# Optimization experiments

Measured on AMD Instinct MI355X. Metric: run time of the kernel, lower is better.

Reference implementation:

```python
import jax, jax.numpy as jnp
import numpy as np
import math

C_CURV = 1.0          # manifold curvature c
KH = KW = 3
STRIDE = (1, 1)
PADDING = (1, 1)
DILATION = (1, 1)
IN_CH = 64            # includes time channel
OUT_CH = 64           # excludes time channel


def setup_inputs() -> dict:
    key = jax.random.key(0)
    k1, k2, k3 = jax.random.split(key, 3)
    B, H, W = 32, 64, 64
    x = jax.random.normal(k1, (B, H, W, IN_CH), dtype=jnp.float32)
    kk = KH * KW
    lin_in = (IN_CH - 1) * kk + 1  # 568
    stdv = math.sqrt(2.0 / ((IN_CH - 1) * kk))
    weight = jax.random.uniform(k2, (OUT_CH, lin_in), minval=-stdv, maxval=stdv, dtype=jnp.float32)
    bias = jax.random.uniform(k3, (OUT_CH,), minval=-stdv, maxval=stdv, dtype=jnp.float32)
    return {"x": x, "weight": weight, "bias": bias}


def _im2col(x):
    """x: [B,H,W,C] -> gathered patches [B,h_out,w_out,KH,KW,C] (torch Unfold semantics)."""
    B, H, W, C = x.shape
    xp = jnp.pad(x, ((0, 0), (PADDING[0], PADDING[0]), (PADDING[1], PADDING[1]), (0, 0)))
    h_out = (H + 2 * PADDING[0] - DILATION[0] * (KH - 1) - 1) // STRIDE[0] + 1
    w_out = (W + 2 * PADDING[1] - DILATION[1] * (KW - 1) - 1) // STRIDE[1] + 1
    rows = STRIDE[0] * jnp.arange(h_out)[:, None] + DILATION[0] * jnp.arange(KH)[None, :]  # [h_out,KH]
    cols = STRIDE[1] * jnp.arange(w_out)[:, None] + DILATION[1] * jnp.arange(KW)[None, :]  # [w_out,KW]
    g = xp[:, rows[:, None, :, None], cols[None, :, None, :], :]  # [B,h_out,w_out,KH,KW,C]
    return g, h_out, w_out


def reference(x, weight, bias):
    B = x.shape[0]
    kk = KH * KW
    g, h_out, w_out = _im2col(x)
    L = h_out * w_out
    # Time channel (channel 0) over kernel positions, clamped to sqrt(c)
    t = jnp.maximum(g[..., 0].reshape(B, L, kk), jnp.sqrt(jnp.float32(C_CURV)))
    t_rescaled = jnp.sqrt(jnp.sum(t * t, axis=-1, keepdims=True) - (kk - 1) * C_CURV)
    # Space channels in kernel-major, channel-minor order (matches torch reshape/transpose)
    s = g[..., 1:].reshape(B, L, kk * (IN_CH - 1))
    feat = jnp.concatenate([t_rescaled, s], axis=-1)  # [B, L, 568]
    # LorentzLinear: linear on features, recompute time from space norm
    y_space = jnp.einsum('blf,of->blo', feat, weight) + bias
    y_time = jnp.sqrt(jnp.sum(y_space * y_space, axis=-1, keepdims=True) + C_CURV)
    out = jnp.concatenate([y_time, y_space], axis=-1)
    return out.reshape(B, h_out, w_out, OUT_CH + 1)
```

## Files before the change

### kernel.cpp

```cpp
#include <hip/hip_runtime.h>
#include <cstdint>
#include <cstddef>

typedef __attribute__((ext_vector_type(8))) short short8v;
typedef __attribute__((ext_vector_type(4))) unsigned uint4v;
typedef __attribute__((ext_vector_type(4))) float floatx4;

#define LIN 568

__device__ __forceinline__ short f32_to_bf16(float f) {
  unsigned u = __builtin_bit_cast(unsigned, f);
  u += 0x7fffu + ((u >> 16) & 1u);
  return (short)(u >> 16);
}
__device__ __forceinline__ float bf16_to_f32(short s) {
  return __builtin_bit_cast(float, ((unsigned)(unsigned short)s) << 16);
}
__device__ __forceinline__ unsigned cvt_pk_bf16(float lo, float hi) {
  unsigned r;
  asm("v_cvt_pk_bf16_f32 %0, %1, %2" : "=v"(r) : "v"(lo), "v"(hi));
  return r;
}

__global__ void prep_weight(const float* __restrict__ w, short* __restrict__ wfragg) {
  int i = blockIdx.x * 256 + threadIdx.x;
  if (i >= 9 * 2 * 4 * 64 * 8) return;
  int j    = i & 7;
  int lane = (i >> 3) & 63;
  int nb   = (i >> 9) & 3;
  int half = (i >> 11) & 1;
  int tap  = i >> 12;
  int n = nb * 16 + (lane & 15);
  int c = half * 32 + ((lane >> 4) << 3) + j;
  float v = (c == 0) ? 0.0f : w[n * LIN + 1 + tap * 63 + (c - 1)];
  wfragg[i] = f32_to_bf16(v);
}

__launch_bounds__(256, 2)
__global__ void lconv_main(const float* __restrict__ x, const float* __restrict__ w,
                           const float* __restrict__ bias, const short* __restrict__ wfragg,
                           float* __restrict__ out) {
  __shared__ short xt[6 * 66 * 72];

  const int tid = threadIdx.x;
  const int bb = blockIdx.x >> 4;
  const int h0 = (blockIdx.x & 15) << 2;
  const float* xb = x + (size_t)bb * (64 * 64 * 64);

  const int lane = tid & 63;
  const int l15 = lane & 15;
  const int q = lane >> 4;
  const int wv = tid >> 6;

  const short* wfl = wfragg + lane * 8;
  short8v b0[4], b1[4], b2[4];
#pragma unroll
  for (int nb = 0; nb < 4; ++nb) {
    b0[nb] = *(const short8v*)(wfl + 0 * 2048 + nb * 512);
    b1[nb] = *(const short8v*)(wfl + 1 * 2048 + nb * 512);
    b2[nb] = *(const short8v*)(wfl + 2 * 2048 + nb * 512);
  }
  float bj[4], w0j[4];
#pragma unroll
  for (int nb = 0; nb < 4; ++nb) {
    int n = nb * 16 + l15;
    bj[nb] = bias[n];
    w0j[nb] = w[n * LIN];
  }

#pragma unroll
  for (int i = 0; i < 8; ++i) {
    int idx = i * 256 + tid;
    int row = idx >> 9;
    int rem = idx & 511;
    int col = rem >> 3;
    int ch8 = (rem & 7) << 3;
    int h = h0 - 1 + row;
    float4 v0 = {0.f, 0.f, 0.f, 0.f}, v1 = {0.f, 0.f, 0.f, 0.f};
    if ((unsigned)h < 64u) {
      const float* p = xb + ((h * 64 + col) * 64 + ch8);
      v0 = *(const float4*)p;
      v1 = *(const float4*)(p + 4);
    }
    uint4v o;
    o[0] = cvt_pk_bf16(v0.x, v0.y);
    o[1] = cvt_pk_bf16(v0.z, v0.w);
    o[2] = cvt_pk_bf16(v1.x, v1.y);
    o[3] = cvt_pk_bf16(v1.z, v1.w);
    *(uint4v*)&xt[(row * 66 + col + 1) * 72 + ch8] = o;
  }
  if (tid < 64) {
    int r = tid >> 4;
    int cc = (tid >> 3) & 1;
    int ch8 = (tid & 7) << 3;
    short8v z = {0, 0, 0, 0, 0, 0, 0, 0};
    *(short8v*)&xt[(r * 66 + cc * 65) * 72 + ch8] = z;
  }
  __syncthreads();

#pragma unroll
  for (int i = 8; i < 12; ++i) {
    int idx = i * 256 + tid;
    int row = idx >> 9;
    int rem = idx & 511;
    int col = rem >> 3;
    int ch8 = (rem & 7) << 3;
    int h = h0 - 1 + row;
    float4 v0 = {0.f, 0.f, 0.f, 0.f}, v1 = {0.f, 0.f, 0.f, 0.f};
    if ((unsigned)h < 64u) {
      const float* p = xb + ((h * 64 + col) * 64 + ch8);
      v0 = *(const float4*)p;
      v1 = *(const float4*)(p + 4);
    }
    uint4v o;
    o[0] = cvt_pk_bf16(v0.x, v0.y);
    o[1] = cvt_pk_bf16(v0.z, v0.w);
    o[2] = cvt_pk_bf16(v1.x, v1.y);
    o[3] = cvt_pk_bf16(v1.z, v1.w);
    *(uint4v*)&xt[(row * 66 + col + 1) * 72 + ch8] = o;
  }
  if (tid < 32) {
    int r = 4 + (tid >> 4);
    int cc = (tid >> 3) & 1;
    int ch8 = (tid & 7) << 3;
    short8v z = {0, 0, 0, 0, 0, 0, 0, 0};
    *(short8v*)&xt[(r * 66 + cc * 65) * 72 + ch8] = z;
  }

  floatx4 acc[4][4];
#pragma unroll
  for (int mb = 0; mb < 4; ++mb)
#pragma unroll
    for (int nb = 0; nb < 4; ++nb) acc[mb][nb] = floatx4{0.f, 0.f, 0.f, 0.f};

  auto do_step = [&](int step) {
    const int tap = step >> 1, half = step & 1;
    const int kh = tap / 3, kw = tap % 3;

    short8v bn[4];
    if (step + 3 < 18) {
#pragma unroll
      for (int nb = 0; nb < 4; ++nb)
        bn[nb] = *(const short8v*)(wfl + (step + 3) * 2048 + nb * 512);
    }

    const short* ab = &xt[((wv + kh) * 66 + kw + l15) * 72 + half * 32 + q * 8];
    short8v a[4];
#pragma unroll
    for (int mb = 0; mb < 4; ++mb)
      a[mb] = *(const short8v*)(ab + mb * 16 * 72);

#pragma unroll
    for (int mb = 0; mb < 4; ++mb) {
#pragma unroll
      for (int nb = 0; nb < 4; ++nb)
        acc[mb][nb] = __builtin_amdgcn_mfma_f32_16x16x32_bf16(a[mb], b0[nb], acc[mb][nb], 0, 0, 0);
    }
#pragma unroll
    for (int nb = 0; nb < 4; ++nb) { b0[nb] = b1[nb]; b1[nb] = b2[nb]; b2[nb] = bn[nb]; }
  };

#pragma unroll
  for (int step = 0; step < 6; ++step) do_step(step);

  __syncthreads();

#pragma unroll
  for (int step = 6; step < 18; ++step) do_step(step);

  float tres_v;
  {
    float ss = 0.f;
#pragma unroll
    for (int dh = 0; dh < 3; ++dh)
#pragma unroll
      for (int dw = 0; dw < 3; ++dw) {
        float tv = bf16_to_f32(xt[((wv + dh) * 66 + lane + dw) * 72]);
        tv = fmaxf(tv, 1.0f);
        ss += tv * tv;
      }
    tres_v = sqrtf(ss - 8.0f);
  }

#pragma unroll
  for (int mb = 0; mb < 4; ++mb) {
#pragma unroll
    for (int r = 0; r < 4; ++r) {
      int pcol = mb * 16 + q * 4 + r;
      float tr = __shfl(tres_v, pcol);
      float v0 = acc[mb][0][r] + bj[0] + tr * w0j[0];
      float v1 = acc[mb][1][r] + bj[1] + tr * w0j[1];
      float v2 = acc[mb][2][r] + bj[2] + tr * w0j[2];
      float v3 = acc[mb][3][r] + bj[3] + tr * w0j[3];
      float ss = v0 * v0 + v1 * v1 + v2 * v2 + v3 * v3;
      ss += __shfl_xor(ss, 1);
      ss += __shfl_xor(ss, 2);
      ss += __shfl_xor(ss, 4);
      ss += __shfl_xor(ss, 8);
      float* ob = out + (size_t)((bb * 64 + h0 + wv) * 64 + pcol) * 65;
      if (l15 == 0) ob[0] = sqrtf(ss + 1.0f);
      ob[1 + l15]  = v0;
      ob[17 + l15] = v1;
      ob[33 + l15] = v2;
      ob[49 + l15] = v3;
    }
  }
}

extern "C" void kernel_launch(void* const* d_in, const int* in_sizes, int n_in,
                              void* d_out, int out_size, void* d_ws, size_t ws_size,
                              hipStream_t stream) {
  const float* x = (const float*)d_in[0];
  const float* w = (const float*)d_in[1];
  const float* b = (const float*)d_in[2];
  float* out = (float*)d_out;
  short* wfragg = (short*)d_ws;

  prep_weight<<<144, 256, 0, stream>>>(w, wfragg);
  lconv_main<<<32 * 16, 256, 0, stream>>>(x, w, b, wfragg, out);
}
```

Before: 98.24 us.

## Split each output row across two waves and swizzle the LDS tile

```diff
diff --git a/kernel.cpp b/kernel.cpp
--- a/kernel.cpp
+++ b/kernel.cpp
@@ -36,11 +36,11 @@
   wfragg[i] = f32_to_bf16(v);
 }
 
-__launch_bounds__(256, 2)
+__launch_bounds__(512, 4)
 __global__ void lconv_main(const float* __restrict__ x, const float* __restrict__ w,
                            const float* __restrict__ bias, const short* __restrict__ wfragg,
                            float* __restrict__ out) {
-  __shared__ short xt[6 * 66 * 72];
+  __shared__ short xt[6 * 64 * 64];
 
   const int tid = threadIdx.x;
   const int bb = blockIdx.x >> 4;
@@ -51,14 +51,15 @@
   const int l15 = lane & 15;
   const int q = lane >> 4;
   const int wv = tid >> 6;
+  const int rr = wv >> 1;
+  const int hw = wv & 1;
 
   const short* wfl = wfragg + lane * 8;
-  short8v b0[4], b1[4], b2[4];
+  short8v b0[4], b1[4];
 #pragma unroll
   for (int nb = 0; nb < 4; ++nb) {
     b0[nb] = *(const short8v*)(wfl + 0 * 2048 + nb * 512);
     b1[nb] = *(const short8v*)(wfl + 1 * 2048 + nb * 512);
-    b2[nb] = *(const short8v*)(wfl + 2 * 2048 + nb * 512);
   }
   float bj[4], w0j[4];
 #pragma unroll
@@ -69,16 +70,16 @@
   }
 
 #pragma unroll
-  for (int i = 0; i < 8; ++i) {
-    int idx = i * 256 + tid;
+  for (int i = 0; i < 4; ++i) {
+    int idx = i * 512 + tid;
     int row = idx >> 9;
     int rem = idx & 511;
     int col = rem >> 3;
-    int ch8 = (rem & 7) << 3;
+    int g   = rem & 7;
     int h = h0 - 1 + row;
     float4 v0 = {0.f, 0.f, 0.f, 0.f}, v1 = {0.f, 0.f, 0.f, 0.f};
     if ((unsigned)h < 64u) {
-      const float* p = xb + ((h * 64 + col) * 64 + ch8);
+      const float* p = xb + ((h * 64 + col) * 64 + g * 8);
       v0 = *(const float4*)p;
       v1 = *(const float4*)(p + 4);
     }
@@ -87,28 +88,21 @@
     o[1] = cvt_pk_bf16(v0.z, v0.w);
     o[2] = cvt_pk_bf16(v1.x, v1.y);
     o[3] = cvt_pk_bf16(v1.z, v1.w);
-    *(uint4v*)&xt[(row * 66 + col + 1) * 72 + ch8] = o;
-  }
-  if (tid < 64) {
-    int r = tid >> 4;
-    int cc = (tid >> 3) & 1;
-    int ch8 = (tid & 7) << 3;
-    short8v z = {0, 0, 0, 0, 0, 0, 0, 0};
-    *(short8v*)&xt[(r * 66 + cc * 65) * 72 + ch8] = z;
+    *(uint4v*)&xt[((row * 64 + col) << 6) + ((g ^ (col & 7)) << 3)] = o;
   }
   __syncthreads();
 
 #pragma unroll
-  for (int i = 8; i < 12; ++i) {
-    int idx = i * 256 + tid;
+  for (int i = 4; i < 6; ++i) {
+    int idx = i * 512 + tid;
     int row = idx >> 9;
     int rem = idx & 511;
     int col = rem >> 3;
-    int ch8 = (rem & 7) << 3;
+    int g   = rem & 7;
     int h = h0 - 1 + row;
     float4 v0 = {0.f, 0.f, 0.f, 0.f}, v1 = {0.f, 0.f, 0.f, 0.f};
     if ((unsigned)h < 64u) {
-      const float* p = xb + ((h * 64 + col) * 64 + ch8);
+      const float* p = xb + ((h * 64 + col) * 64 + g * 8);
       v0 = *(const float4*)p;
       v1 = *(const float4*)(p + 4);
     }
@@ -117,19 +111,12 @@
     o[1] = cvt_pk_bf16(v0.z, v0.w);
     o[2] = cvt_pk_bf16(v1.x, v1.y);
     o[3] = cvt_pk_bf16(v1.z, v1.w);
-    *(uint4v*)&xt[(row * 66 + col + 1) * 72 + ch8] = o;
-  }
-  if (tid < 32) {
-    int r = 4 + (tid >> 4);
-    int cc = (tid >> 3) & 1;
-    int ch8 = (tid & 7) << 3;
-    short8v z = {0, 0, 0, 0, 0, 0, 0, 0};
-    *(short8v*)&xt[(r * 66 + cc * 65) * 72 + ch8] = z;
-  }
-
-  floatx4 acc[4][4];
-#pragma unroll
-  for (int mb = 0; mb < 4; ++mb)
+    *(uint4v*)&xt[((row * 64 + col) << 6) + ((g ^ (col & 7)) << 3)] = o;
+  }
+
+  floatx4 acc[2][4];
+#pragma unroll
+  for (int mb = 0; mb < 2; ++mb)
 #pragma unroll
     for (int nb = 0; nb < 4; ++nb) acc[mb][nb] = floatx4{0.f, 0.f, 0.f, 0.f};
 
@@ -138,26 +125,33 @@
     const int kh = tap / 3, kw = tap % 3;
 
     short8v bn[4];
-    if (step + 3 < 18) {
+    if (step + 2 < 18) {
 #pragma unroll
       for (int nb = 0; nb < 4; ++nb)
-        bn[nb] = *(const short8v*)(wfl + (step + 3) * 2048 + nb * 512);
-    }
-
-    const short* ab = &xt[((wv + kh) * 66 + kw + l15) * 72 + half * 32 + q * 8];
-    short8v a[4];
-#pragma unroll
-    for (int mb = 0; mb < 4; ++mb)
-      a[mb] = *(const short8v*)(ab + mb * 16 * 72);
-
-#pragma unroll
-    for (int mb = 0; mb < 4; ++mb) {
+        bn[nb] = *(const short8v*)(wfl + (step + 2) * 2048 + nb * 512);
+    }
+
+    const int rb = (rr + kh) << 6;
+    const int cb = l15 + kw - 1;
+    const int ch = (half << 2) + q;
+    short8v a[2];
+#pragma unroll
+    for (int mb = 0; mb < 2; ++mb) {
+      int col = (cb + (hw * 2 + mb) * 16) & 63;
+      a[mb] = *(const short8v*)&xt[((rb + col) << 6) + ((ch ^ (col & 7)) << 3)];
+    }
+    short8v z = {0, 0, 0, 0, 0, 0, 0, 0};
+    if (kw == 0 && hw == 0 && l15 == 0)  a[0] = z;
+    if (kw == 2 && hw == 1 && l15 == 15) a[1] = z;
+
+#pragma unroll
+    for (int mb = 0; mb < 2; ++mb) {
 #pragma unroll
       for (int nb = 0; nb < 4; ++nb)
         acc[mb][nb] = __builtin_amdgcn_mfma_f32_16x16x32_bf16(a[mb], b0[nb], acc[mb][nb], 0, 0, 0);
     }
 #pragma unroll
-    for (int nb = 0; nb < 4; ++nb) { b0[nb] = b1[nb]; b1[nb] = b2[nb]; b2[nb] = bn[nb]; }
+    for (int nb = 0; nb < 4; ++nb) { b0[nb] = b1[nb]; b1[nb] = bn[nb]; }
   };
 
 #pragma unroll
@@ -170,12 +164,16 @@
 
   float tres_v;
   {
+    int pc = hw * 32 + (lane & 31);
     float ss = 0.f;
 #pragma unroll
     for (int dh = 0; dh < 3; ++dh)
 #pragma unroll
       for (int dw = 0; dw < 3; ++dw) {
-        float tv = bf16_to_f32(xt[((wv + dh) * 66 + lane + dw) * 72]);
+        int c = pc + dw - 1;
+        int cc = c & 63;
+        float tv = bf16_to_f32(xt[(((rr + dh) * 64 + cc) << 6) + ((cc & 7) << 3)]);
+        tv = ((unsigned)c < 64u) ? tv : 0.f;
         tv = fmaxf(tv, 1.0f);
         ss += tv * tv;
       }
@@ -183,11 +181,11 @@
   }
 
 #pragma unroll
-  for (int mb = 0; mb < 4; ++mb) {
+  for (int mb = 0; mb < 2; ++mb) {
 #pragma unroll
     for (int r = 0; r < 4; ++r) {
-      int pcol = mb * 16 + q * 4 + r;
-      float tr = __shfl(tres_v, pcol);
+      int pcol = (hw * 2 + mb) * 16 + q * 4 + r;
+      float tr = __shfl(tres_v, mb * 16 + q * 4 + r);
       float v0 = acc[mb][0][r] + bj[0] + tr * w0j[0];
       float v1 = acc[mb][1][r] + bj[1] + tr * w0j[1];
       float v2 = acc[mb][2][r] + bj[2] + tr * w0j[2];
@@ -197,7 +195,7 @@
       ss += __shfl_xor(ss, 2);
       ss += __shfl_xor(ss, 4);
       ss += __shfl_xor(ss, 8);
-      float* ob = out + (size_t)((bb * 64 + h0 + wv) * 64 + pcol) * 65;
+      float* ob = out + (size_t)((bb * 64 + h0 + rr) * 64 + pcol) * 65;
       if (l15 == 0) ob[0] = sqrtf(ss + 1.0f);
       ob[1 + l15]  = v0;
       ob[17 + l15] = v1;
@@ -217,5 +215,5 @@
   short* wfragg = (short*)d_ws;
 
   prep_weight<<<144, 256, 0, stream>>>(w, wfragg);
-  lconv_main<<<32 * 16, 256, 0, stream>>>(x, w, b, wfragg, out);
-}
+  lconv_main<<<32 * 16, 512, 0, stream>>>(x, w, b, wfragg, out);
+}
```

Result: slower. 105.3 us (+7.2%).

## Prefetch all input tiles up front, overlap conversion with MFMA, use DPP reductions

Applied to the files above, without the earlier changes.

```diff
diff --git a/kernel.cpp b/kernel.cpp
--- a/kernel.cpp
+++ b/kernel.cpp
@@ -20,6 +20,11 @@
   unsigned r;
   asm("v_cvt_pk_bf16_f32 %0, %1, %2" : "=v"(r) : "v"(lo), "v"(hi));
   return r;
+}
+template<int CTRL>
+__device__ __forceinline__ float dpp_add(float v) {
+  int y = __builtin_amdgcn_update_dpp(0, __builtin_bit_cast(int, v), CTRL, 0xF, 0xF, true);
+  return v + __builtin_bit_cast(float, y);
 }
 
 __global__ void prep_weight(const float* __restrict__ w, short* __restrict__ wfragg) {
@@ -41,6 +46,7 @@
                            const float* __restrict__ bias, const short* __restrict__ wfragg,
                            float* __restrict__ out) {
   __shared__ short xt[6 * 66 * 72];
+  __shared__ float tres_s[4 * 64];
 
   const int tid = threadIdx.x;
   const int bb = blockIdx.x >> 4;
@@ -51,6 +57,24 @@
   const int l15 = lane & 15;
   const int q = lane >> 4;
   const int wv = tid >> 6;
+
+  float4 s0[12], s1[12];
+#pragma unroll
+  for (int i = 0; i < 12; ++i) {
+    int idx = i * 256 + tid;
+    int row = idx >> 9;
+    int rem = idx & 511;
+    int col = rem >> 3;
+    int ch8 = (rem & 7) << 3;
+    int h = h0 - 1 + row;
+    s0[i] = {0.f, 0.f, 0.f, 0.f};
+    s1[i] = {0.f, 0.f, 0.f, 0.f};
+    if ((unsigned)h < 64u) {
+      const float* p = xb + ((h * 64 + col) * 64 + ch8);
+      s0[i] = *(const float4*)p;
+      s1[i] = *(const float4*)(p + 4);
+    }
+  }
 
   const short* wfl = wfragg + lane * 8;
   short8v b0[4], b1[4], b2[4];
@@ -75,18 +99,11 @@
     int rem = idx & 511;
     int col = rem >> 3;
     int ch8 = (rem & 7) << 3;
-    int h = h0 - 1 + row;
-    float4 v0 = {0.f, 0.f, 0.f, 0.f}, v1 = {0.f, 0.f, 0.f, 0.f};
-    if ((unsigned)h < 64u) {
-      const float* p = xb + ((h * 64 + col) * 64 + ch8);
-      v0 = *(const float4*)p;
-      v1 = *(const float4*)(p + 4);
-    }
     uint4v o;
-    o[0] = cvt_pk_bf16(v0.x, v0.y);
-    o[1] = cvt_pk_bf16(v0.z, v0.w);
-    o[2] = cvt_pk_bf16(v1.x, v1.y);
-    o[3] = cvt_pk_bf16(v1.z, v1.w);
+    o[0] = cvt_pk_bf16(s0[i].x, s0[i].y);
+    o[1] = cvt_pk_bf16(s0[i].z, s0[i].w);
+    o[2] = cvt_pk_bf16(s1[i].x, s1[i].y);
+    o[3] = cvt_pk_bf16(s1[i].z, s1[i].w);
     *(uint4v*)&xt[(row * 66 + col + 1) * 72 + ch8] = o;
   }
   if (tid < 64) {
@@ -98,6 +115,42 @@
   }
   __syncthreads();
 
+  floatx4 acc[4][4];
+#pragma unroll
+  for (int mb = 0; mb < 4; ++mb)
+#pragma unroll
+    for (int nb = 0; nb < 4; ++nb) acc[mb][nb] = floatx4{0.f, 0.f, 0.f, 0.f};
+
+  auto do_step = [&](int step) {
+    const int tap = step >> 1, half = step & 1;
+    const int kh = tap / 3, kw = tap % 3;
+
+    short8v bn[4];
+    if (step + 3 < 18) {
+#pragma unroll
+      for (int nb = 0; nb < 4; ++nb)
+        bn[nb] = *(const short8v*)(wfl + (step + 3) * 2048 + nb * 512);
+    }
+
+    const short* ab = &xt[((wv + kh) * 66 + kw + l15) * 72 + half * 32 + q * 8];
+    short8v a[4];
+#pragma unroll
+    for (int mb = 0; mb < 4; ++mb)
+      a[mb] = *(const short8v*)(ab + mb * 16 * 72);
+
+#pragma unroll
+    for (int mb = 0; mb < 4; ++mb) {
+#pragma unroll
+      for (int nb = 0; nb < 4; ++nb)
+        acc[mb][nb] = __builtin_amdgcn_mfma_f32_16x16x32_bf16(a[mb], b0[nb], acc[mb][nb], 0, 0, 0);
+    }
+#pragma unroll
+    for (int nb = 0; nb < 4; ++nb) { b0[nb] = b1[nb]; b1[nb] = b2[nb]; b2[nb] = bn[nb]; }
+  };
+
+#pragma unroll
+  for (int step = 0; step < 6; ++step) do_step(step);
+
 #pragma unroll
   for (int i = 8; i < 12; ++i) {
     int idx = i * 256 + tid;
@@ -105,18 +158,11 @@
     int rem = idx & 511;
     int col = rem >> 3;
     int ch8 = (rem & 7) << 3;
-    int h = h0 - 1 + row;
-    float4 v0 = {0.f, 0.f, 0.f, 0.f}, v1 = {0.f, 0.f, 0.f, 0.f};
-    if ((unsigned)h < 64u) {
-      const float* p = xb + ((h * 64 + col) * 64 + ch8);
-      v0 = *(const float4*)p;
-      v1 = *(const float4*)(p + 4);
-    }
     uint4v o;
-    o[0] = cvt_pk_bf16(v0.x, v0.y);
-    o[1] = cvt_pk_bf16(v0.z, v0.w);
-    o[2] = cvt_pk_bf16(v1.x, v1.y);
-    o[3] = cvt_pk_bf16(v1.z, v1.w);
+    o[0] = cvt_pk_bf16(s0[i].x, s0[i].y);
+    o[1] = cvt_pk_bf16(s0[i].z, s0[i].w);
+    o[2] = cvt_pk_bf16(s1[i].x, s1[i].y);
+    o[3] = cvt_pk_bf16(s1[i].z, s1[i].w);
     *(uint4v*)&xt[(row * 66 + col + 1) * 72 + ch8] = o;
   }
   if (tid < 32) {
@@ -126,49 +172,11 @@
     short8v z = {0, 0, 0, 0, 0, 0, 0, 0};
     *(short8v*)&xt[(r * 66 + cc * 65) * 72 + ch8] = z;
   }
-
-  floatx4 acc[4][4];
-#pragma unroll
-  for (int mb = 0; mb < 4; ++mb)
-#pragma unroll
-    for (int nb = 0; nb < 4; ++nb) acc[mb][nb] = floatx4{0.f, 0.f, 0.f, 0.f};
-
-  auto do_step = [&](int step) {
-    const int tap = step >> 1, half = step & 1;
-    const int kh = tap / 3, kw = tap % 3;
-
-    short8v bn[4];
-    if (step + 3 < 18) {
-#pragma unroll
-      for (int nb = 0; nb < 4; ++nb)
-        bn[nb] = *(const short8v*)(wfl + (step + 3) * 2048 + nb * 512);
-    }
-
-    const short* ab = &xt[((wv + kh) * 66 + kw + l15) * 72 + half * 32 + q * 8];
-    short8v a[4];
-#pragma unroll
-    for (int mb = 0; mb < 4; ++mb)
-      a[mb] = *(const short8v*)(ab + mb * 16 * 72);
-
-#pragma unroll
-    for (int mb = 0; mb < 4; ++mb) {
-#pragma unroll
-      for (int nb = 0; nb < 4; ++nb)
-        acc[mb][nb] = __builtin_amdgcn_mfma_f32_16x16x32_bf16(a[mb], b0[nb], acc[mb][nb], 0, 0, 0);
-    }
-#pragma unroll
-    for (int nb = 0; nb < 4; ++nb) { b0[nb] = b1[nb]; b1[nb] = b2[nb]; b2[nb] = bn[nb]; }
-  };
-
-#pragma unroll
-  for (int step = 0; step < 6; ++step) do_step(step);
-
   __syncthreads();
 
 #pragma unroll
   for (int step = 6; step < 18; ++step) do_step(step);
 
-  float tres_v;
   {
     float ss = 0.f;
 #pragma unroll
@@ -179,24 +187,25 @@
         tv = fmaxf(tv, 1.0f);
         ss += tv * tv;
       }
-    tres_v = sqrtf(ss - 8.0f);
+    tres_s[wv * 64 + lane] = sqrtf(ss - 8.0f);
   }
 
 #pragma unroll
   for (int mb = 0; mb < 4; ++mb) {
+    float4 t4 = *(const float4*)&tres_s[wv * 64 + mb * 16 + q * 4];
 #pragma unroll
     for (int r = 0; r < 4; ++r) {
       int pcol = mb * 16 + q * 4 + r;
-      float tr = __shfl(tres_v, pcol);
+      float tr = t4[r];
       float v0 = acc[mb][0][r] + bj[0] + tr * w0j[0];
       float v1 = acc[mb][1][r] + bj[1] + tr * w0j[1];
       float v2 = acc[mb][2][r] + bj[2] + tr * w0j[2];
       float v3 = acc[mb][3][r] + bj[3] + tr * w0j[3];
       float ss = v0 * v0 + v1 * v1 + v2 * v2 + v3 * v3;
-      ss += __shfl_xor(ss, 1);
-      ss += __shfl_xor(ss, 2);
-      ss += __shfl_xor(ss, 4);
-      ss += __shfl_xor(ss, 8);
+      ss = dpp_add<0xB1>(ss);
+      ss = dpp_add<0x4E>(ss);
+      ss = dpp_add<0x141>(ss);
+      ss = dpp_add<0x140>(ss);
       float* ob = out + (size_t)((bb * 64 + h0 + wv) * 64 + pcol) * 65;
       if (l15 == 0) ob[0] = sqrtf(ss + 1.0f);
       ob[1 + l15]  = v0;
```

Measured after the change: 96.47 us. Within noise of the previous version (-1.8%).
